# Performance work log

Hardware: AMD Instinct MI355X
Metric: run time of the kernel (lower is better)

The kernel has to match this reference:

```python
import jax, jax.numpy as jnp
import numpy as np

B = 262144      # parallel environments / batch
N_IN = 4        # sensory neurons (hardcoded n_inputs=4 in TWC)
N_HID = 64      # hidden interneurons
N_OUT = 8       # output/motor neurons
N_EDGES = 128   # sparse gap-junction edges in->hid
STEPS = 4       # internal_steps


def setup_inputs() -> dict:
    key = jax.random.key(0)
    ks = jax.random.split(key, 18)
    rn = lambda k, s, sc=1.0: jax.random.normal(k, s, dtype=jnp.float32) * sc
    return {
        'x':           rn(ks[0], (B, N_IN)),
        'hid_E0':      rn(ks[1], (B, N_HID), 0.1),
        'hid_O0':      rn(ks[2], (B, N_HID), 0.1),
        'out_E0':      rn(ks[3], (B, N_OUT), 0.1),
        'out_O0':      rn(ks[4], (B, N_OUT), 0.1),
        'w_in2hid_IN': rn(ks[5], (N_IN, N_HID), 0.1),
        'w_hid_IN':    rn(ks[6], (N_HID, N_HID), 0.1),
        'w_hid_EX':    rn(ks[7], (N_HID, N_HID), 0.1),
        'w_hid2out':   rn(ks[8], (N_HID, N_OUT), 0.1),
        'gj_w':        rn(ks[9], (N_EDGES,), 0.1),
        'th_in':       rn(ks[10], (N_IN,), 0.1),
        'dec_in':      jax.random.uniform(ks[11], (N_IN,), dtype=jnp.float32),
        'th_hid':      rn(ks[12], (N_HID,), 0.1),
        'dec_hid':     jax.random.uniform(ks[13], (N_HID,), dtype=jnp.float32),
        'th_out':      rn(ks[14], (N_OUT,), 0.1),
        'dec_out':     jax.random.uniform(ks[15], (N_OUT,), dtype=jnp.float32),
        'gj_src':      jax.random.randint(ks[16], (N_EDGES,), 0, N_IN, dtype=jnp.int32),
        'gj_dst':      jax.random.randint(ks[17], (N_EDGES,), 0, N_HID, dtype=jnp.int32),
    }


def _gate(E, th):
    # FIURI neuron output: pass internal state when above threshold, else 0
    return jnp.where(E >= th, E, jnp.zeros_like(E))


def reference(x, hid_E0, hid_O0, out_E0, out_O0,
              w_in2hid_IN, w_hid_IN, w_hid_EX, w_hid2out, gj_w,
              th_in, dec_in, th_hid, dec_hid, th_out, dec_out,
              gj_src, gj_dst):
    sp = jax.nn.softplus
    # obs encoder: ex_in + in_in == x (passthrough split into +/- parts)
    o_in_pre = x                              # in_O used for all connections
    # input layer neuron_step on state (x, x): leak only, no external input
    E_in = dec_in * x                         # [B, N_IN]
    O_in = _gate(E_in, th_in)

    # loop-invariant dense influences (TWC uses the ORIGINAL hid O each iter)
    in2hid = -(o_in_pre @ sp(w_in2hid_IN))    # inhibitory dense conn [B,N_HID]
    hid2hid = hid_O0 @ (sp(w_hid_EX) - sp(w_hid_IN))  # EX + IN dense conns
    # sparse gap junction: I_gj[b,j] = sum_e sp(gj_w[e])*(o_pre[b,src]-E[b,dst])
    sw = sp(gj_w)
    M = jnp.zeros((N_IN, N_HID), x.dtype).at[gj_src, gj_dst].add(sw)
    deg = jnp.zeros((N_HID,), x.dtype).at[gj_dst].add(sw)
    gj_in = o_in_pre @ M                      # [B, N_HID], loop-invariant part
    I_const = in2hid + hid2hid + gj_in

    E_hid, O_hid = hid_E0, hid_O0
    for _ in range(STEPS):
        E_hid = dec_hid * E_hid + I_const - deg * E_hid
        O_hid = _gate(E_hid, th_hid)

    # output layer driven by the ORIGINAL hid O (per TWC._recurrent_step)
    h2o = hid_O0 @ sp(w_hid2out)              # excitatory dense conn [B,N_OUT]
    E_out = dec_out * out_E0 + h2o
    O_out = _gate(E_out, th_out)
    action = jnp.tanh(E_out)                  # action_decoder on internal E
    return (action, E_in, O_in, E_hid, O_hid, E_out, O_out)
```

## Files before the change

### kernel.cpp

```cpp
#include <hip/hip_runtime.h>
#include <math.h>

#define NT 256
#define RPB 64

typedef __attribute__((ext_vector_type(8))) short bf16x8;
typedef __attribute__((ext_vector_type(4))) float f32x4;

__device__ __forceinline__ float softplus_f(float v) {
    return fmaxf(v, 0.0f) + log1pf(expf(-fabsf(v)));
}
__device__ __forceinline__ unsigned short bfr(float f) {
    unsigned int u = __float_as_uint(f);
    u += 0x7FFFu + ((u >> 16) & 1u);
    return (unsigned short)(u >> 16);
}
__device__ __forceinline__ unsigned int bfpack(float a, float b) {
    return (unsigned int)bfr(a) | ((unsigned int)bfr(b) << 16);
}
__device__ __forceinline__ void nt_store4(float4* p, float4 v) {
    f32x4 nv = { v.x, v.y, v.z, v.w };
    __builtin_nontemporal_store(nv, reinterpret_cast<f32x4*>(p));
}
__device__ __forceinline__ void nt_store1(float* p, float v) {
    __builtin_nontemporal_store(v, p);
}


__global__ __launch_bounds__(NT) void twc_prep(
    const float* __restrict__ w_in2hid,
    const float* __restrict__ w_hid_IN,
    const float* __restrict__ w_hid_EX,
    const float* __restrict__ w_hid2out,
    const float* __restrict__ gj_w,
    const float* __restrict__ th_in,
    const float* __restrict__ dec_in,
    const float* __restrict__ th_hid,
    const float* __restrict__ dec_hid,
    const float* __restrict__ th_out,
    const float* __restrict__ dec_out,
    const int* __restrict__ gj_src,
    const int* __restrict__ gj_dst,
    float* __restrict__ ws)
{
    const int t = threadIdx.x;
    const int blk = blockIdx.x;
    unsigned short* wsS = (unsigned short*)ws;
    if (blk < 30) {
        const int e = blk * NT + t;
        const int col = e / 96, k = e - col * 96;
        if (col < 64 && k >= 64 && k < 68) return;
        float v = 0.0f;
        if (col < 64 && k < 64)
            v = softplus_f(w_hid_EX[k * 64 + col]) - softplus_f(w_hid_IN[k * 64 + col]);
        else if (col >= 64 && col < 72 && k < 64)
            v = softplus_f(w_hid2out[k * 8 + (col - 64)]);
        wsS[e] = bfr(v);
    } else {
        __shared__ float sw[128];
        __shared__ int ssrc[128], sdst[128];
        if (t < 128) { sw[t] = softplus_f(gj_w[t]); ssrc[t] = gj_src[t]; sdst[t] = gj_dst[t]; }
        __syncthreads();
        if (t < 64) {
            const int j = t;
            float m0 = 0.f, m1 = 0.f, m2 = 0.f, m3 = 0.f, deg = 0.f;
            #pragma unroll 4
            for (int e = 0; e < 128; ++e) {
                const float w = (sdst[e] == j) ? sw[e] : 0.0f;
                deg += w;
                const int se = ssrc[e];
                m0 += (se == 0) ? w : 0.0f;
                m1 += (se == 1) ? w : 0.0f;
                m2 += (se == 2) ? w : 0.0f;
                m3 += (se == 3) ? w : 0.0f;
            }
            wsS[j * 96 + 64] = bfr(m0 - softplus_f(w_in2hid[0 * 64 + j]));
            wsS[j * 96 + 65] = bfr(m1 - softplus_f(w_in2hid[1 * 64 + j]));
            wsS[j * 96 + 66] = bfr(m2 - softplus_f(w_in2hid[2 * 64 + j]));
            wsS[j * 96 + 67] = bfr(m3 - softplus_f(w_in2hid[3 * 64 + j]));
            const float a  = dec_hid[j] - deg;
            const float a2 = a * a;
            ws[3840 + j] = a2 * a2;
            ws[3904 + j] = 1.0f + a + a2 + a2 * a;
            ws[3968 + j] = th_hid[j];
        }
        if (t < 4) { ws[4032 + t] = dec_in[t];  ws[4036 + t] = th_in[t]; }
        if (t < 8) { ws[4040 + t] = dec_out[t]; ws[4048 + t] = th_out[t]; }
    }
}

__global__ __launch_bounds__(NT, 4) void twc_main(
    const float* __restrict__ x,
    const float* __restrict__ hidE0,
    const float* __restrict__ hidO0,
    const float* __restrict__ outE0,
    const float* __restrict__ ws,
    float* __restrict__ out, int B)
{
    __shared__ __align__(16) float buf[64 * 76];
    const int t = threadIdx.x;
    const int l = t & 63, w = t >> 6;
    const int fr = l & 15, lg = l >> 4;
    const size_t rowBase = (size_t)blockIdx.x * RPB;
    const size_t Bs = (size_t)B;
    float4* out4 = (float4*)out;
    const float* wsf = ws;

    float4 e0pre[4];
    float eo0pre[2];
    {
        const float4* gE0 = (const float4*)hidE0 + rowBase * 16;
        #pragma unroll
        for (int j = 0; j < 4; ++j) e0pre[j] = gE0[j * NT + t];
        #pragma unroll
        for (int j = 0; j < 2; ++j) eo0pre[j] = outE0[rowBase * 8 + j * NT + t];
    }

    const int arow = w * 16 + fr;
    bf16x8 af0, af1, af2;
    {
        const float4* gO0r = (const float4*)hidO0 + (rowBase + arow) * 16;
        const float4 v0 = gO0r[lg * 2],     v1 = gO0r[lg * 2 + 1];
        const float4 v2 = gO0r[8 + lg * 2], v3 = gO0r[8 + lg * 2 + 1];
        unsigned int a0[4] = { bfpack(v0.x, v0.y), bfpack(v0.z, v0.w),
                               bfpack(v1.x, v1.y), bfpack(v1.z, v1.w) };
        unsigned int a1[4] = { bfpack(v2.x, v2.y), bfpack(v2.z, v2.w),
                               bfpack(v3.x, v3.y), bfpack(v3.z, v3.w) };
        af0 = *(const bf16x8*)a0;
        af1 = *(const bf16x8*)a1;
        unsigned int a2[4] = { 0u, 0u, 0u, 0u };
        if (lg == 0) {
            const float4 xr = ((const float4*)x)[rowBase + arow];
            a2[0] = bfpack(xr.x, xr.y);
            a2[1] = bfpack(xr.z, xr.w);
        }
        af2 = *(const bf16x8*)a2;
    }

    if (t < 64) {
        const float4 xv = ((const float4*)x)[rowBase + t];
        const float4 di = ((const float4*)ws)[1008];
        const float4 ti = ((const float4*)ws)[1009];
        float4 Ein, Oin;
        Ein.x = di.x * xv.x; Ein.y = di.y * xv.y; Ein.z = di.z * xv.z; Ein.w = di.w * xv.w;
        Oin.x = (Ein.x >= ti.x) ? Ein.x : 0.0f;
        Oin.y = (Ein.y >= ti.y) ? Ein.y : 0.0f;
        Oin.z = (Ein.z >= ti.z) ? Ein.z : 0.0f;
        Oin.w = (Ein.w >= ti.w) ? Ein.w : 0.0f;
        nt_store4(&out4[Bs * 2 + rowBase + t], Ein);
        nt_store4(&out4[Bs * 3 + rowBase + t], Oin);
    }

    f32x4 acc[5];
    {
        const f32x4 z = {0.0f, 0.0f, 0.0f, 0.0f};
        #pragma unroll
        for (int ct = 0; ct < 5; ++ct) acc[ct] = z;
        const bf16x8* wsB = (const bf16x8*)ws;
        #pragma unroll
        for (int ct = 0; ct < 5; ++ct) {
            const int cb = (ct * 16 + fr) * 12 + lg;
            acc[ct] = __builtin_amdgcn_mfma_f32_16x16x32_bf16(af0, wsB[cb],     acc[ct], 0, 0, 0);
            acc[ct] = __builtin_amdgcn_mfma_f32_16x16x32_bf16(af1, wsB[cb + 4], acc[ct], 0, 0, 0);
            acc[ct] = __builtin_amdgcn_mfma_f32_16x16x32_bf16(af2, wsB[cb + 8], acc[ct], 0, 0, 0);
        }
    }

    {
        const int rowl = w * 16 + lg * 4;
        #pragma unroll
        for (int ct = 0; ct < 4; ++ct) {
            const int c = ct * 16 + fr;
            const float qs = wsf[3904 + c];
            #pragma unroll
            for (int r = 0; r < 4; ++r)
                buf[(rowl + r) * 76 + c] = qs * acc[ct][r];
        }
        if (fr < 8) {
            #pragma unroll
            for (int r = 0; r < 4; ++r)
                buf[(rowl + r) * 76 + 64 + fr] = acc[4][r];
        }
    }
    __syncthreads();

    {
        const float4* th4 = (const float4*)ws + 992;
        const float4* p44 = (const float4*)ws + 960;
        #pragma unroll
        for (int j = 0; j < 4; ++j) {
            const int i = j * NT + t;
            const int row = i >> 4, c4 = i & 15;
            const float4 qi = *(const float4*)&buf[row * 76 + c4 * 4];
            const float4 p4 = p44[c4];
            const float4 e0 = e0pre[j];
            const float4 th = th4[c4];
            float4 E, O;
            E.x = fmaf(p4.x, e0.x, qi.x);
            E.y = fmaf(p4.y, e0.y, qi.y);
            E.z = fmaf(p4.z, e0.z, qi.z);
            E.w = fmaf(p4.w, e0.w, qi.w);
            O.x = (E.x >= th.x) ? E.x : 0.0f;
            O.y = (E.y >= th.y) ? E.y : 0.0f;
            O.z = (E.z >= th.z) ? E.z : 0.0f;
            O.w = (E.w >= th.w) ? E.w : 0.0f;
            nt_store4(&out4[Bs * 4  + rowBase * 16 + i], E);
            nt_store4(&out4[Bs * 20 + rowBase * 16 + i], O);
        }
        #pragma unroll
        for (int j = 0; j < 2; ++j) {
            const int idx = j * NT + t;
            const int row = idx >> 3, q = idx & 7;
            const float h  = buf[row * 76 + 64 + q];
            const float eo = fmaf(wsf[4040 + q], eo0pre[j], h);
            nt_store1(&out[rowBase * 8 + idx], tanhf(eo));
            nt_store1(&out[Bs * 144 + rowBase * 8 + idx], eo);
            nt_store1(&out[Bs * 152 + rowBase * 8 + idx], (eo >= wsf[4048 + q]) ? eo : 0.0f);
        }
    }
}

extern "C" void kernel_launch(void* const* d_in, const int* in_sizes, int n_in,
                              void* d_out, int out_size, void* d_ws, size_t ws_size,
                              hipStream_t stream) {
    (void)n_in; (void)out_size; (void)ws_size;
    const float* x        = (const float*)d_in[0];
    const float* hidE0    = (const float*)d_in[1];
    const float* hidO0    = (const float*)d_in[2];
    const float* outE0    = (const float*)d_in[3];
    const float* w_in2hid = (const float*)d_in[5];
    const float* w_hid_IN = (const float*)d_in[6];
    const float* w_hid_EX = (const float*)d_in[7];
    const float* w_hid2out= (const float*)d_in[8];
    const float* gj_w     = (const float*)d_in[9];
    const float* th_in    = (const float*)d_in[10];
    const float* dec_in   = (const float*)d_in[11];
    const float* th_hid   = (const float*)d_in[12];
    const float* dec_hid  = (const float*)d_in[13];
    const float* th_out   = (const float*)d_in[14];
    const float* dec_out  = (const float*)d_in[15];
    const int*   gj_src   = (const int*)d_in[16];
    const int*   gj_dst   = (const int*)d_in[17];
    float* out = (float*)d_out;
    float* ws  = (float*)d_ws;

    const int B = in_sizes[0] / 4;

    twc_prep<<<31, NT, 0, stream>>>(
        w_in2hid, w_hid_IN, w_hid_EX, w_hid2out, gj_w,
        th_in, dec_in, th_hid, dec_hid, th_out, dec_out,
        gj_src, gj_dst, ws);

    twc_main<<<B / RPB, NT, 0, stream>>>(x, hidE0, hidO0, outE0, ws, out, B);
}
```

Before: 67.88 us.

## Process two 64-row tiles per block, reusing B fragments across MFMAs

Each block now handles 128 rows instead of 64. Every thread loads A fragments for two row tiles and issues MFMAs for both against the same loaded weight fragments, which halves weight loads per row and halves the block count. The epilogue runs twice through the shared buffer, with extra barriers between the two passes. Register use roughly doubles, so launch bounds drop to 2 blocks per SM, which lowers occupancy on a memory-bound kernel.

```diff
diff --git a/kernel.cpp b/kernel.cpp
--- a/kernel.cpp
+++ b/kernel.cpp
@@ -2,7 +2,7 @@
 #include <math.h>
 
 #define NT 256
-#define RPB 64
+#define RPB 128
 
 typedef __attribute__((ext_vector_type(8))) short bf16x8;
 typedef __attribute__((ext_vector_type(4))) float f32x4;
@@ -89,7 +89,7 @@
     }
 }
 
-__global__ __launch_bounds__(NT, 4) void twc_main(
+__global__ __launch_bounds__(NT, 2) void twc_main(
     const float* __restrict__ x,
     const float* __restrict__ hidE0,
     const float* __restrict__ hidO0,
@@ -106,38 +106,47 @@
     float4* out4 = (float4*)out;
     const float* wsf = ws;
 
-    float4 e0pre[4];
-    float eo0pre[2];
+    float4 e0pre[8];
+    float eo0pre[4];
     {
         const float4* gE0 = (const float4*)hidE0 + rowBase * 16;
         #pragma unroll
-        for (int j = 0; j < 4; ++j) e0pre[j] = gE0[j * NT + t];
-        #pragma unroll
-        for (int j = 0; j < 2; ++j) eo0pre[j] = outE0[rowBase * 8 + j * NT + t];
+        for (int j = 0; j < 8; ++j) e0pre[j] = gE0[j * NT + t];
+        #pragma unroll
+        for (int j = 0; j < 4; ++j) eo0pre[j] = outE0[rowBase * 8 + j * NT + t];
     }
 
     const int arow = w * 16 + fr;
-    bf16x8 af0, af1, af2;
-    {
-        const float4* gO0r = (const float4*)hidO0 + (rowBase + arow) * 16;
-        const float4 v0 = gO0r[lg * 2],     v1 = gO0r[lg * 2 + 1];
-        const float4 v2 = gO0r[8 + lg * 2], v3 = gO0r[8 + lg * 2 + 1];
-        unsigned int a0[4] = { bfpack(v0.x, v0.y), bfpack(v0.z, v0.w),
+    bf16x8 a0s0, a0s1, a0s2, a1s0, a1s1, a1s2;
+    {
+        const float4* g0 = (const float4*)hidO0 + (rowBase + arow) * 16;
+        const float4* g1 = (const float4*)hidO0 + (rowBase + 64 + arow) * 16;
+        const float4 u0 = g0[lg * 2],     u1 = g0[lg * 2 + 1];
+        const float4 u2 = g0[8 + lg * 2], u3 = g0[8 + lg * 2 + 1];
+        const float4 v0 = g1[lg * 2],     v1 = g1[lg * 2 + 1];
+        const float4 v2 = g1[8 + lg * 2], v3 = g1[8 + lg * 2 + 1];
+        unsigned int p0[4] = { bfpack(u0.x, u0.y), bfpack(u0.z, u0.w),
+                               bfpack(u1.x, u1.y), bfpack(u1.z, u1.w) };
+        unsigned int p1[4] = { bfpack(u2.x, u2.y), bfpack(u2.z, u2.w),
+                               bfpack(u3.x, u3.y), bfpack(u3.z, u3.w) };
+        unsigned int p2[4] = { bfpack(v0.x, v0.y), bfpack(v0.z, v0.w),
                                bfpack(v1.x, v1.y), bfpack(v1.z, v1.w) };
-        unsigned int a1[4] = { bfpack(v2.x, v2.y), bfpack(v2.z, v2.w),
+        unsigned int p3[4] = { bfpack(v2.x, v2.y), bfpack(v2.z, v2.w),
                                bfpack(v3.x, v3.y), bfpack(v3.z, v3.w) };
-        af0 = *(const bf16x8*)a0;
-        af1 = *(const bf16x8*)a1;
-        unsigned int a2[4] = { 0u, 0u, 0u, 0u };
+        a0s0 = *(const bf16x8*)p0;  a0s1 = *(const bf16x8*)p1;
+        a1s0 = *(const bf16x8*)p2;  a1s1 = *(const bf16x8*)p3;
+        unsigned int q0[4] = { 0u, 0u, 0u, 0u };
+        unsigned int q1[4] = { 0u, 0u, 0u, 0u };
         if (lg == 0) {
-            const float4 xr = ((const float4*)x)[rowBase + arow];
-            a2[0] = bfpack(xr.x, xr.y);
-            a2[1] = bfpack(xr.z, xr.w);
-        }
-        af2 = *(const bf16x8*)a2;
-    }
-
-    if (t < 64) {
+            const float4 x0 = ((const float4*)x)[rowBase + arow];
+            const float4 x1 = ((const float4*)x)[rowBase + 64 + arow];
+            q0[0] = bfpack(x0.x, x0.y);  q0[1] = bfpack(x0.z, x0.w);
+            q1[0] = bfpack(x1.x, x1.y);  q1[1] = bfpack(x1.z, x1.w);
+        }
+        a0s2 = *(const bf16x8*)q0;  a1s2 = *(const bf16x8*)q1;
+    }
+
+    if (t < 128) {
         const float4 xv = ((const float4*)x)[rowBase + t];
         const float4 di = ((const float4*)ws)[1008];
         const float4 ti = ((const float4*)ws)[1009];
@@ -151,42 +160,46 @@
         nt_store4(&out4[Bs * 3 + rowBase + t], Oin);
     }
 
-    f32x4 acc[5];
+    f32x4 acc0[5], acc1[5];
     {
         const f32x4 z = {0.0f, 0.0f, 0.0f, 0.0f};
         #pragma unroll
-        for (int ct = 0; ct < 5; ++ct) acc[ct] = z;
+        for (int ct = 0; ct < 5; ++ct) { acc0[ct] = z; acc1[ct] = z; }
         const bf16x8* wsB = (const bf16x8*)ws;
         #pragma unroll
         for (int ct = 0; ct < 5; ++ct) {
             const int cb = (ct * 16 + fr) * 12 + lg;
-            acc[ct] = __builtin_amdgcn_mfma_f32_16x16x32_bf16(af0, wsB[cb],     acc[ct], 0, 0, 0);
-            acc[ct] = __builtin_amdgcn_mfma_f32_16x16x32_bf16(af1, wsB[cb + 4], acc[ct], 0, 0, 0);
-            acc[ct] = __builtin_amdgcn_mfma_f32_16x16x32_bf16(af2, wsB[cb + 8], acc[ct], 0, 0, 0);
-        }
-    }
-
-    {
-        const int rowl = w * 16 + lg * 4;
+            const bf16x8 b0 = wsB[cb], b1 = wsB[cb + 4], b2 = wsB[cb + 8];
+            acc0[ct] = __builtin_amdgcn_mfma_f32_16x16x32_bf16(a0s0, b0, acc0[ct], 0, 0, 0);
+            acc0[ct] = __builtin_amdgcn_mfma_f32_16x16x32_bf16(a0s1, b1, acc0[ct], 0, 0, 0);
+            acc0[ct] = __builtin_amdgcn_mfma_f32_16x16x32_bf16(a0s2, b2, acc0[ct], 0, 0, 0);
+            acc1[ct] = __builtin_amdgcn_mfma_f32_16x16x32_bf16(a1s0, b0, acc1[ct], 0, 0, 0);
+            acc1[ct] = __builtin_amdgcn_mfma_f32_16x16x32_bf16(a1s1, b1, acc1[ct], 0, 0, 0);
+            acc1[ct] = __builtin_amdgcn_mfma_f32_16x16x32_bf16(a1s2, b2, acc1[ct], 0, 0, 0);
+        }
+    }
+
+    const float4* th4 = (const float4*)ws + 992;
+    const float4* p44 = (const float4*)ws + 960;
+    const int rowl = w * 16 + lg * 4;
+
+    {
         #pragma unroll
         for (int ct = 0; ct < 4; ++ct) {
             const int c = ct * 16 + fr;
             const float qs = wsf[3904 + c];
             #pragma unroll
             for (int r = 0; r < 4; ++r)
-                buf[(rowl + r) * 76 + c] = qs * acc[ct][r];
+                buf[(rowl + r) * 76 + c] = qs * acc0[ct][r];
         }
         if (fr < 8) {
             #pragma unroll
             for (int r = 0; r < 4; ++r)
-                buf[(rowl + r) * 76 + 64 + fr] = acc[4][r];
+                buf[(rowl + r) * 76 + 64 + fr] = acc0[4][r];
         }
     }
     __syncthreads();
-
-    {
-        const float4* th4 = (const float4*)ws + 992;
-        const float4* p44 = (const float4*)ws + 960;
+    {
         #pragma unroll
         for (int j = 0; j < 4; ++j) {
             const int i = j * NT + t;
@@ -216,6 +229,57 @@
             nt_store1(&out[rowBase * 8 + idx], tanhf(eo));
             nt_store1(&out[Bs * 144 + rowBase * 8 + idx], eo);
             nt_store1(&out[Bs * 152 + rowBase * 8 + idx], (eo >= wsf[4048 + q]) ? eo : 0.0f);
+        }
+    }
+    __syncthreads();
+
+    {
+        #pragma unroll
+        for (int ct = 0; ct < 4; ++ct) {
+            const int c = ct * 16 + fr;
+            const float qs = wsf[3904 + c];
+            #pragma unroll
+            for (int r = 0; r < 4; ++r)
+                buf[(rowl + r) * 76 + c] = qs * acc1[ct][r];
+        }
+        if (fr < 8) {
+            #pragma unroll
+            for (int r = 0; r < 4; ++r)
+                buf[(rowl + r) * 76 + 64 + fr] = acc1[4][r];
+        }
+    }
+    __syncthreads();
+    {
+        const size_t rb1 = rowBase + 64;
+        #pragma unroll
+        for (int j = 0; j < 4; ++j) {
+            const int i = j * NT + t;
+            const int row = i >> 4, c4 = i & 15;
+            const float4 qi = *(const float4*)&buf[row * 76 + c4 * 4];
+            const float4 p4 = p44[c4];
+            const float4 e0 = e0pre[4 + j];
+            const float4 th = th4[c4];
+            float4 E, O;
+            E.x = fmaf(p4.x, e0.x, qi.x);
+            E.y = fmaf(p4.y, e0.y, qi.y);
+            E.z = fmaf(p4.z, e0.z, qi.z);
+            E.w = fmaf(p4.w, e0.w, qi.w);
+            O.x = (E.x >= th.x) ? E.x : 0.0f;
+            O.y = (E.y >= th.y) ? E.y : 0.0f;
+            O.z = (E.z >= th.z) ? E.z : 0.0f;
+            O.w = (E.w >= th.w) ? E.w : 0.0f;
+            nt_store4(&out4[Bs * 4  + rb1 * 16 + i], E);
+            nt_store4(&out4[Bs * 20 + rb1 * 16 + i], O);
+        }
+        #pragma unroll
+        for (int j = 0; j < 2; ++j) {
+            const int idx = j * NT + t;
+            const int row = idx >> 3, q = idx & 7;
+            const float h  = buf[row * 76 + 64 + q];
+            const float eo = fmaf(wsf[4040 + q], eo0pre[2 + j], h);
+            nt_store1(&out[rb1 * 8 + idx], tanhf(eo));
+            nt_store1(&out[Bs * 144 + rb1 * 8 + idx], eo);
+            nt_store1(&out[Bs * 152 + rb1 * 8 + idx], (eo >= wsf[4048 + q]) ? eo : 0.0f);
         }
     }
 }
```

Result: faster. 65.63 us (-3.3%).
